# Kernel tuning notes

Measured on AMD Instinct MI355X. Metric: run time of the kernel, lower is better.

Reference implementation:

```python
import jax, jax.numpy as jnp
import numpy as np

B, Tin, Tout = 256, 32, 29
Venc, Vdec = 29, 72
E = 256; H = 256; L = 3; G = 4 * H; D = 2 * L  # bidirectional dirs * layers


def lstm_step(x, h, c, Wih0, Wih1, Whh, b):
    """One timestep of a 3-layer bidirectional LSTM (torch gate order i,f,g,o).
    x: [B, in], h/c: [D, B, H] in torch layout (layer-major, dir-minor)."""
    new_h, new_c = [], []
    inp = x
    for l in range(L):
        outs = []
        for d in range(2):
            idx = 2 * l + d
            Wih = Wih0[d] if l == 0 else Wih1[l - 1, d]
            g = inp @ Wih.T + h[idx] @ Whh[l, d].T + b[l, d]
            i_g, f_g, g_g, o_g = jnp.split(g, 4, axis=-1)
            cc = jax.nn.sigmoid(f_g) * c[idx] + jax.nn.sigmoid(i_g) * jnp.tanh(g_g)
            hh = jax.nn.sigmoid(o_g) * jnp.tanh(cc)
            new_h.append(hh); new_c.append(cc); outs.append(hh)
        inp = jnp.concatenate(outs, axis=-1)  # feeds next layer: [B, 2H]
    return jnp.stack(new_h), jnp.stack(new_c), inp


def proj(hid, W1, b1, W2, b2):
    """Linear over hidden dim then Linear over the layer*dir dim -- the exact
    math of torch's linear1 -> permute(2,1,0) -> linear2 -> permute(2,1,0)."""
    hn = jnp.einsum('lbh,gh->lbg', hid, W1) + b1            # [D, B, H]
    return jnp.einsum('lbh,ml->mbh', hn, W2) + b2[:, None, None]


def setup_inputs() -> dict:
    key = jax.random.key(0)
    ks = iter(jax.random.split(key, 64))
    def p(shape, scale=0.06):
        return jax.random.normal(next(ks), shape, jnp.float32) * scale
    return {
        "input": jax.random.randint(next(ks), (B, Tin), 0, Venc),
        "target": jax.random.randint(next(ks), (B, Tout), 0, Vdec),
        "teacher_force": 1,
        "enc_emb": p((Venc, E)), "dec_emb": p((Vdec, E)),
        "enc_Wih0": p((2, G, E)), "enc_Wih1": p((L - 1, 2, G, 2 * H)),
        "enc_Whh": p((L, 2, G, H)), "enc_b": p((L, 2, G)),
        "dec_Wih0": p((2, G, E)), "dec_Wih1": p((L - 1, 2, G, 2 * H)),
        "dec_Whh": p((L, 2, G, H)), "dec_b": p((L, 2, G)),
        "lin_h_W1": p((H, H)), "lin_h_b1": p((H,)), "lin_h_W2": p((D, D)), "lin_h_b2": p((D,)),
        "lin_c_W1": p((H, H)), "lin_c_b1": p((H,)), "lin_c_W2": p((D, D)), "lin_c_b2": p((D,)),
        "lin_a_W1": p((H, H)), "lin_a_b1": p((H,)), "lin_a_W2": p((D, D)), "lin_a_b2": p((D,)),
        "attn_W": p((E, E + H)), "attn_b": p((E,)),
        "fc_W": p((Vdec, 2 * H)), "fc_b": p((Vdec,)),
    }


def reference(input, target, teacher_force, enc_emb, dec_emb, enc_Wih0, enc_Wih1, enc_Whh, enc_b, dec_Wih0, dec_Wih1, dec_Whh, dec_b, lin_h_W1, lin_h_b1, lin_h_W2, lin_h_b2, lin_c_W1, lin_c_b1, lin_c_W2, lin_c_b2, lin_a_W1, lin_a_b1, lin_a_W2, lin_a_b2, attn_W, attn_b, fc_W, fc_b):
    Bb = input.shape[0]
    h0 = jnp.zeros((D, Bb, H), jnp.float32)

    # ---- encoder: step LSTM over Tin, projecting hidden per step for attention ----
    def enc_step(carry, x_t):
        h, c = carry
        h, c, _ = lstm_step(enc_emb[x_t], h, c, enc_Wih0, enc_Wih1, enc_Whh, enc_b)
        return (h, c), proj(h, lin_a_W1, lin_a_b1, lin_a_W2, lin_a_b2)

    (h, c), encoder_outputs = jax.lax.scan(enc_step, (h0, h0), input.T)  # [Tin, D, B, H]

    # ---- encoder->decoder state bridging (linear over H, linear over D) ----
    dec_h = proj(h, lin_h_W1, lin_h_b1, lin_h_W2, lin_h_b2)
    dec_c = proj(c, lin_c_W1, lin_c_b1, lin_c_W2, lin_c_b2)

    def dec_core(h, c, tok):
        emb = dec_emb[tok]                                # [B, E]
        energies = h[None] * encoder_outputs              # [Tin, D, B, H]
        aw = jax.nn.softmax(energies, axis=0)             # attn over source time
        ctx = (aw * encoder_outputs).sum(0).mean(0)       # [B, H]
        x = jnp.concatenate([emb, ctx], -1) @ attn_W.T + attn_b
        h, c, top = lstm_step(x, h, c, dec_Wih0, dec_Wih1, dec_Whh, dec_b)
        return h, c, top @ fc_W.T + fc_b, aw.sum(-1)      # logits [B,V], aw [Tin,D,B]

    if teacher_force:
        def step(carry, tok):
            h, c = carry
            h, c, logits, _ = dec_core(h, c, tok)
            return (h, c), logits
        _, logits_seq = jax.lax.scan(step, (dec_h, dec_c), target[:, :Tout - 1].T)
        attn_seq = jnp.zeros((Tout - 1, Tin, D, Bb), jnp.float32)
    else:
        def step(carry, _):
            h, c, tok = carry
            h, c, logits, aw = dec_core(h, c, tok)
            nxt = jnp.argmax(jax.nn.softmax(logits, -1), -1).astype(tok.dtype)
            return (h, c, nxt), (logits, aw)
        tok0 = jnp.ones((Bb,), input.dtype)
        _, (logits_seq, attn_seq) = jax.lax.scan(step, (dec_h, dec_c, tok0), None, length=Tout - 1)

    pred0 = jnp.zeros((1, Bb, Vdec), jnp.float32).at[0, :, 1].set(1.0)
    predicted = jnp.concatenate([pred0, logits_seq], 0)   # [Tout, B, Vdec]
    attn_weights = jnp.concatenate([jnp.zeros((1, Tin, D, Bb), jnp.float32), attn_seq], 0)
    return predicted, attn_weights
```

## Files before the change

kernel.cpp:

```cpp
#include <hip/hip_runtime.h>
#include <math.h>

#define BB 256
#define TIN 32
#define TOUT 29
#define VDEC 72
#define EDIM 256
#define HDIM 256
#define DD 6
#define BH (BB*HDIM)

typedef unsigned short u16;
typedef unsigned int u32;
typedef __bf16 bf16x8 __attribute__((ext_vector_type(8)));
typedef float f32x4 __attribute__((ext_vector_type(4)));
typedef u16 u16x8 __attribute__((ext_vector_type(8)));

__device__ __forceinline__ float sigmf(float x){ return 1.0f/(1.0f+__expf(-x)); }
__device__ __forceinline__ float tanhf_fast(float x){ return 1.0f - 2.0f/(1.0f+__expf(2.0f*x)); }
__device__ __forceinline__ u16 f2bf(float f){
  u32 u = __builtin_bit_cast(u32, f);
  u32 r = (u + 0x7fffu + ((u>>16)&1u)) >> 16;
  return (u16)r;
}
__device__ __forceinline__ float bf2f(u16 s){
  u32 u = ((u32)s)<<16; return __builtin_bit_cast(float, u);
}
__device__ __forceinline__ bf16x8 ldbf8(const u16* p){
  u16x8 t = *(const u16x8*)p; return __builtin_bit_cast(bf16x8, t);
}
__device__ __forceinline__ f32x4 mfma16(bf16x8 a, bf16x8 b, f32x4 c){
  return __builtin_amdgcn_mfma_f32_16x16x32_bf16(a, b, c, 0, 0, 0);
}

__global__ void fill_zero_u32(u32* __restrict__ p, int n){
  int i = blockIdx.x*256 + threadIdx.x;
  if (i < n) p[i] = 0u;
}

__global__ void init_out_kernel(float* __restrict__ out, int n){
  int i = blockIdx.x*256 + threadIdx.x;
  if (i >= n) return;
  float v = 0.0f;
  if (i < BB*VDEC && (i % VDEC) == 1) v = 1.0f;
  out[i] = v;
}

__global__ void bias2d_kernel(const float* __restrict__ W2a, const float* __restrict__ b1a, const float* __restrict__ b2a,
                              const float* __restrict__ W2h, const float* __restrict__ b1h, const float* __restrict__ b2h,
                              const float* __restrict__ W2c, const float* __restrict__ b1c, const float* __restrict__ b2c,
                              float* __restrict__ outp){
  int g = threadIdx.x;
  const float* W2[3] = {W2a, W2h, W2c};
  const float* b1[3] = {b1a, b1h, b1c};
  const float* b2[3] = {b2a, b2h, b2c};
  for (int p = 0; p < 3; p++)
    for (int m = 0; m < 6; m++){
      float s = 0.f;
      for (int l = 0; l < 6; l++) s += W2[p][m*6+l];
      outp[p*1536 + m*256 + g] = s * b1[p][g] + b2[p][m];
    }
}

__global__ void embed_enc_kernel(const int* __restrict__ input, const float* __restrict__ enc_emb,
                                 u16* __restrict__ x_emb){
  int i = blockIdx.x*256 + threadIdx.x;
  int e = i & 255, b = (i >> 8) & 255, t = i >> 16;
  x_emb[i] = f2bf(enc_emb[(size_t)input[b*TIN + t]*EDIM + e]);
}

__global__ void pack_w_kernel(const float* __restrict__ Wih, const float* __restrict__ Whh,
                              u16* __restrict__ dst, int K1, int K){
  int k = blockIdx.x*256 + threadIdx.x;
  int row = blockIdx.y;
  int d = row >> 10, rr = row & 1023;
  int ht = rr >> 6, r = rr & 63;
  int g = (r>>4)*256 + ht*16 + (r&15);
  float v;
  if (k < K1) v = Wih[((size_t)d*1024 + g)*K1 + k];
  else        v = Whh[((size_t)d*1024 + g)*256 + (k - K1)];
  dst[(size_t)row*K + k] = f2bf(v);
}

__global__ void pack_wfused_kernel(const float* __restrict__ Wih0, const float* __restrict__ attn_W,
                                   const float* __restrict__ Whh, u16* __restrict__ dst){
  int k = blockIdx.x*256 + threadIdx.x;
  int row = blockIdx.y;
  int d = row >> 10, rr = row & 1023;
  int ht = rr >> 6, r = rr & 63;
  int g = (r>>4)*256 + ht*16 + (r&15);
  float v;
  if (k >= 512) v = Whh[((size_t)d*1024 + g)*256 + (k - 512)];
  else {
    const float* wr = Wih0 + ((size_t)d*1024 + g)*256;
    float s = 0.f;
    #pragma unroll 4
    for (int o = 0; o < 256; o++) s += wr[o] * attn_W[(size_t)o*512 + k];
    v = s;
  }
  dst[(size_t)row*768 + k] = f2bf(v);
}

__global__ void biasfold_kernel(const float* __restrict__ Wih0, const float* __restrict__ attn_b,
                                const float* __restrict__ dec_b, float* __restrict__ outb){
  int i = blockIdx.x*256 + threadIdx.x;
  int d = i >> 10, g = i & 1023;
  const float* wr = Wih0 + ((size_t)d*1024 + g)*256;
  float s = dec_b[d*1024 + g];
  #pragma unroll 4
  for (int o = 0; o < 256; o++) s += wr[o]*attn_b[o];
  outb[i] = s;
}

__global__ void mix_kernel(const float* __restrict__ inp, float* __restrict__ outp,
                           const float* __restrict__ W2, int n){
  int i = blockIdx.x*256 + threadIdx.x;
  if (i >= n) return;
  int h = i & 255, b = (i >> 8) & 255, t = i >> 16;
  size_t base = ((size_t)t*6)*BH + (size_t)b*256 + h;
  float v[6];
  #pragma unroll
  for (int l = 0; l < 6; l++) v[l] = inp[base + (size_t)l*BH];
  #pragma unroll
  for (int m = 0; m < 6; m++){
    float s = 0.f;
    #pragma unroll
    for (int l = 0; l < 6; l++) s += W2[m*6+l]*v[l];
    outp[base + (size_t)m*BH] = s;
  }
}

__global__ __launch_bounds__(256) void gemmN256_kernel(const float* __restrict__ A, float* __restrict__ C,
                                                       const float* __restrict__ W,
                                                       const float* __restrict__ bias2d,
                                                       u16* __restrict__ Cbf){
  __shared__ float As[32][33];
  __shared__ float Ws[256][34];
  int tid = threadIdx.x;
  int m_base = blockIdx.x * 32;
  int rg = tid >> 5, cg = tid & 31;
  float acc[4][8];
  #pragma unroll
  for (int i=0;i<4;i++)
    #pragma unroll
    for (int j=0;j<8;j++) acc[i][j]=0.f;
  for (int k0 = 0; k0 < 256; k0 += 32){
    #pragma unroll
    for (int p=0;p<4;p++) As[rg + p*8][cg] = A[(size_t)(m_base + rg + p*8)*256 + k0 + cg];
    #pragma unroll
    for (int p=0;p<32;p++) Ws[rg + p*8][cg] = W[(size_t)(rg + p*8)*256 + k0 + cg];
    __syncthreads();
    #pragma unroll
    for (int kk=0; kk<32; kk++){
      float a[4], w[8];
      #pragma unroll
      for (int i=0;i<4;i++) a[i] = As[rg*4+i][kk];
      #pragma unroll
      for (int j=0;j<8;j++) w[j] = Ws[cg*8+j][kk];
      #pragma unroll
      for (int i=0;i<4;i++)
        #pragma unroll
        for (int j=0;j<8;j++) acc[i][j] += a[i]*w[j];
    }
    __syncthreads();
  }
  #pragma unroll
  for (int i=0;i<4;i++){
    int row = m_base + rg*4 + i;
    int bm = (row >> 8) % 6;
    #pragma unroll
    for (int j=0;j<8;j++){
      float v = acc[i][j] + bias2d[bm*256 + cg*8 + j];
      if (C)   C[(size_t)row*256 + cg*8 + j] = v;
      if (Cbf) Cbf[(size_t)row*256 + cg*8 + j] = f2bf(v);
    }
  }
}

template<int K1>
__global__ __launch_bounds__(256) void lstm_stage_mfma(
    const u16* __restrict__ inp,
    const u16* __restrict__ Wpk,
    const float* __restrict__ bias_l,
    const u16* __restrict__ hR, u16* __restrict__ hW,
    float* __restrict__ cBuf, u16* __restrict__ inp_out,
    float* __restrict__ h_all_t, int l){
  constexpr int K = K1 + 256;
  constexpr int NIT = K >> 6;
  __shared__ __align__(16) u16 As[2][32][72];
  __shared__ __align__(16) u16 Ws[2][64][72];
  __shared__ float Gt[4][32][17];
  int tid = threadIdx.x;
  int m_base = blockIdx.x*32;
  int d = blockIdx.y >> 4, ht = blockIdx.y & 15;
  int idx = 2*l + d;
  const u16* Wblk = Wpk + (size_t)((d*16+ht)*64)*K;
  int q = tid >> 6, lane = tid & 63;
  int ar = tid >> 3, kp = (tid & 7)*8;
  const u16* aRow  = inp + (size_t)(m_base+ar)*K1 + kp;
  const u16* hRow  = hR + (size_t)idx*BH + (size_t)(m_base+ar)*HDIM + kp - K1;
  const u16* wRow0 = Wblk + (size_t)ar*K + kp;
  const u16* wRow1 = Wblk + (size_t)(ar+32)*K + kp;
  uint4 aP[2], w0P[2], w1P[2];
  #pragma unroll
  for (int pf = 0; pf < 2; pf++){
    int c0 = pf*64;
    const u16* ap = (c0 + kp < K1) ? aRow : hRow;
    aP[pf]  = *(const uint4*)(ap + c0);
    w0P[pf] = *(const uint4*)(wRow0 + c0);
    w1P[pf] = *(const uint4*)(wRow1 + c0);
  }
  f32x4 acc0 = {0.f,0.f,0.f,0.f}, acc1 = {0.f,0.f,0.f,0.f};
  #pragma unroll
  for (int i = 0; i < NIT; i++){
    int p = i & 1;
    *(uint4*)&As[p][ar][kp]     = aP[p];
    *(uint4*)&Ws[p][ar][kp]     = w0P[p];
    *(uint4*)&Ws[p][ar+32][kp]  = w1P[p];
    int c0n = (i+2) << 6;
    if (c0n < K){
      const u16* ap = (c0n + kp < K1) ? aRow : hRow;
      aP[p]  = *(const uint4*)(ap + c0n);
      w0P[p] = *(const uint4*)(wRow0 + c0n);
      w1P[p] = *(const uint4*)(wRow1 + c0n);
    }
    __syncthreads();
    #pragma unroll
    for (int kh = 0; kh < 2; kh++){
      int kb = kh*32 + (lane>>4)*8;
      bf16x8 a0 = ldbf8(&As[p][lane & 15][kb]);
      bf16x8 a1 = ldbf8(&As[p][16 + (lane & 15)][kb]);
      bf16x8 bq = ldbf8(&Ws[p][q*16 + (lane & 15)][kb]);
      acc0 = mfma16(a0, bq, acc0);
      acc1 = mfma16(a1, bq, acc1);
    }
  }
  int hh = lane & 15, rq = lane >> 4;
  #pragma unroll
  for (int r = 0; r < 4; r++){
    Gt[q][rq*4 + r][hh]      = acc0[r];
    Gt[q][16 + rq*4 + r][hh] = acc1[r];
  }
  __syncthreads();
  const float* bias = bias_l + d*1024;
  #pragma unroll
  for (int it = 0; it < 2; it++){
    int id = tid + it*256;
    int bb = id >> 4, h2 = id & 15;
    int b = m_base + bb, h = ht*16 + h2;
    float iv = Gt[0][bb][h2] + bias[h];
    float fv = Gt[1][bb][h2] + bias[256 + h];
    float gv = Gt[2][bb][h2] + bias[512 + h];
    float ov = Gt[3][bb][h2] + bias[768 + h];
    size_t off = (size_t)idx*BH + (size_t)b*HDIM + h;
    float cold = cBuf[off];
    float cc = sigmf(fv)*cold + sigmf(iv)*tanhf_fast(gv);
    float hv = sigmf(ov)*tanhf_fast(cc);
    cBuf[off] = cc;
    u16 hb = f2bf(hv);
    hW[off] = hb;
    inp_out[(size_t)b*512 + d*HDIM + h] = hb;
    if (h_all_t) h_all_t[off] = hv;
  }
}

__global__ void attn_tok_kernel(const u16* __restrict__ hR, const u16* __restrict__ eo,
                                u16* __restrict__ cat, const int* __restrict__ tf,
                                float* __restrict__ attn_out, int step,
                                const int* __restrict__ target, float* __restrict__ outp,
                                const float* __restrict__ dec_emb, const u16* __restrict__ top,
                                const float* __restrict__ fc_W, const float* __restrict__ fc_b){
  int blk = blockIdx.x, tid = threadIdx.x;
  __shared__ float s[512];
  __shared__ float lg[VDEC];
  __shared__ int tokS;
  if (blk < 256){
    int b = blk, hc = tid;
    bool wa = (tf[0] == 0);
    float acc = 0.f;
    for (int d = 0; d < DD; d++){
      float hv = bf2f(hR[(size_t)d*BH + (size_t)b*256 + hc]);
      const u16* ep = eo + (size_t)d*BH + (size_t)b*256 + hc;
      float se = 0.f, ac = 0.f;
      #pragma unroll 8
      for (int t = 0; t < TIN; t++){
        float ev = bf2f(ep[(size_t)t*(DD*BH)]);
        float e = __expf(hv*ev);
        se += e; ac += e*ev;
      }
      acc += ac/se;
      if (wa){
        float inv = 1.f/se;
        for (int t = 0; t < TIN; t++){
          float ev = bf2f(ep[(size_t)t*(DD*BH)]);
          atomicAdd(&attn_out[(((size_t)(step+1)*TIN + t)*DD + d)*BB + b], __expf(hv*ev)*inv);
        }
      }
    }
    cat[(size_t)b*512 + 256 + hc] = f2bf(acc*(1.0f/6.0f));
  } else {
    int b = blk - 256;
    if (step > 0){
      s[tid]       = bf2f(top[(size_t)b*512 + tid]);
      s[tid + 256] = bf2f(top[(size_t)b*512 + 256 + tid]);
      __syncthreads();
      if (tid < VDEC){
        float a = fc_b[tid];
        #pragma unroll 4
        for (int k = 0; k < 512; k++) a += s[k]*fc_W[(size_t)tid*512 + k];
        outp[((size_t)step*BB + b)*VDEC + tid] = a;
        lg[tid] = a;
      }
      __syncthreads();
    }
    int tok;
    if (tf[0]) tok = target[b*TOUT + step];
    else if (step == 0) tok = 1;
    else {
      if (tid == 0){
        int bi = 0; float bv = lg[0];
        for (int v = 1; v < VDEC; v++){ float x = lg[v]; if (x > bv){ bv = x; bi = v; } }
        tokS = bi;
      }
      __syncthreads();
      tok = tokS;
    }
    cat[(size_t)b*512 + tid] = f2bf(dec_emb[(size_t)tok*EDIM + tid]);
  }
}

__global__ void fc_kernel(const u16* __restrict__ top, const float* __restrict__ fc_W,
                          const float* __restrict__ fc_b, float* __restrict__ outp, int step){
  __shared__ float s[512];
  int b = blockIdx.x, tid = threadIdx.x;
  s[tid]       = bf2f(top[(size_t)b*512 + tid]);
  s[tid + 256] = bf2f(top[(size_t)b*512 + 256 + tid]);
  __syncthreads();
  if (tid < VDEC){
    float a = fc_b[tid];
    #pragma unroll 4
    for (int k = 0; k < 512; k++) a += s[k]*fc_W[(size_t)tid*512 + k];
    outp[((size_t)(step+1)*BB + b)*VDEC + tid] = a;
  }
}


extern "C" void kernel_launch(void* const* d_in, const int* in_sizes, int n_in,
                              void* d_out, int out_size, void* d_ws, size_t ws_size,
                              hipStream_t stream){
  (void)in_sizes; (void)n_in; (void)out_size; (void)ws_size;
  const int*   input    = (const int*)d_in[0];
  const int*   target   = (const int*)d_in[1];
  const int*   tf       = (const int*)d_in[2];
  const float* enc_emb  = (const float*)d_in[3];
  const float* dec_emb  = (const float*)d_in[4];
  const float* enc_Wih0 = (const float*)d_in[5];
  const float* enc_Wih1 = (const float*)d_in[6];
  const float* enc_Whh  = (const float*)d_in[7];
  const float* enc_b    = (const float*)d_in[8];
  const float* dec_Wih0 = (const float*)d_in[9];
  const float* dec_Wih1 = (const float*)d_in[10];
  const float* dec_Whh  = (const float*)d_in[11];
  const float* dec_b    = (const float*)d_in[12];
  const float* lin_h_W1 = (const float*)d_in[13];
  const float* lin_h_b1 = (const float*)d_in[14];
  const float* lin_h_W2 = (const float*)d_in[15];
  const float* lin_h_b2 = (const float*)d_in[16];
  const float* lin_c_W1 = (const float*)d_in[17];
  const float* lin_c_b1 = (const float*)d_in[18];
  const float* lin_c_W2 = (const float*)d_in[19];
  const float* lin_c_b2 = (const float*)d_in[20];
  const float* lin_a_W1 = (const float*)d_in[21];
  const float* lin_a_b1 = (const float*)d_in[22];
  const float* lin_a_W2 = (const float*)d_in[23];
  const float* lin_a_b2 = (const float*)d_in[24];
  const float* attn_W   = (const float*)d_in[25];
  const float* attn_b   = (const float*)d_in[26];
  const float* fc_W     = (const float*)d_in[27];
  const float* fc_b     = (const float*)d_in[28];
  float* out = (float*)d_out;

  char* base = (char*)d_ws;
  size_t off = 0;
  auto alloc = [&](size_t bytes)->char*{
    char* p = base + off; off += (bytes + 255) & ~(size_t)255; return p;
  };
  float* h_all  = (float*)alloc(sizeof(float)*(size_t)TIN*DD*BH);
  float* tmp6   = (float*)alloc(sizeof(float)*(size_t)DD*BH);
  float* dec_c  = (float*)alloc(sizeof(float)*(size_t)DD*BH);
  float* bias2d = (float*)alloc(sizeof(float)*3*6*256);
  u16*   enc_hA = (u16*)alloc(sizeof(u16)*(size_t)DD*BH + sizeof(float)*(size_t)DD*BH);
  float* enc_c  = (float*)(enc_hA + (size_t)DD*BH);
  u16* enc_hB = (u16*)alloc(sizeof(u16)*(size_t)DD*BH);
  u16* dec_hA = (u16*)alloc(sizeof(u16)*(size_t)DD*BH);
  u16* dec_hB = (u16*)alloc(sizeof(u16)*(size_t)DD*BH);
  u16* x_emb  = (u16*)alloc(sizeof(u16)*(size_t)TIN*BB*EDIM);
  u16* bufA   = (u16*)alloc(sizeof(u16)*(size_t)BB*512);
  u16* bufB   = (u16*)alloc(sizeof(u16)*(size_t)BB*512);
  u16* cat    = (u16*)alloc(sizeof(u16)*(size_t)BB*512);
  u16* eo_bf  = (u16*)alloc(sizeof(u16)*(size_t)TIN*DD*BH);
  u16* wp_e0  = (u16*)alloc(sizeof(u16)*(size_t)2048*512);
  u16* wp_e1  = (u16*)alloc(sizeof(u16)*(size_t)2048*768);
  u16* wp_e2  = (u16*)alloc(sizeof(u16)*(size_t)2048*768);
  u16* wp_d0f = (u16*)alloc(sizeof(u16)*(size_t)2048*768);
  u16* wp_d1  = (u16*)alloc(sizeof(u16)*(size_t)2048*768);
  u16* wp_d2  = (u16*)alloc(sizeof(u16)*(size_t)2048*768);
  float* fb0  = (float*)alloc(sizeof(float)*2048);

  const int outn = TOUT*BB*VDEC + TOUT*TIN*DD*BB;
  init_out_kernel<<<(outn+255)/256, 256, 0, stream>>>(out, outn);
  fill_zero_u32<<<(DD*BH*6/4 + 255)/256, 256, 0, stream>>>((u32*)enc_hA, DD*BH*6/4);
  bias2d_kernel<<<1, 256, 0, stream>>>(lin_a_W2, lin_a_b1, lin_a_b2,
                                       lin_h_W2, lin_h_b1, lin_h_b2,
                                       lin_c_W2, lin_c_b1, lin_c_b2, bias2d);
  embed_enc_kernel<<<(TIN*BB*EDIM)/256, 256, 0, stream>>>(input, enc_emb, x_emb);
  pack_w_kernel<<<dim3(2,2048), 256, 0, stream>>>(enc_Wih0, enc_Whh,                       wp_e0, 256, 512);
  pack_w_kernel<<<dim3(3,2048), 256, 0, stream>>>(enc_Wih1, enc_Whh + 2*1024*256,          wp_e1, 512, 768);
  pack_w_kernel<<<dim3(3,2048), 256, 0, stream>>>(enc_Wih1 + (size_t)2*1024*512, enc_Whh + 4*1024*256, wp_e2, 512, 768);
  pack_wfused_kernel<<<dim3(3,2048), 256, 0, stream>>>(dec_Wih0, attn_W, dec_Whh,          wp_d0f);
  biasfold_kernel<<<8, 256, 0, stream>>>(dec_Wih0, attn_b, dec_b, fb0);
  pack_w_kernel<<<dim3(3,2048), 256, 0, stream>>>(dec_Wih1, dec_Whh + 2*1024*256,          wp_d1, 512, 768);
  pack_w_kernel<<<dim3(3,2048), 256, 0, stream>>>(dec_Wih1 + (size_t)2*1024*512, dec_Whh + 4*1024*256, wp_d2, 512, 768);

  dim3 sgrid(8, 32);
  for (int t = 0; t < TIN; t++){
    const u16* hRb = (t & 1) ? enc_hB : enc_hA;
    u16*       hWb = (t & 1) ? enc_hA : enc_hB;
    float* hat = h_all + (size_t)t*DD*BH;
    lstm_stage_mfma<256><<<sgrid,256,0,stream>>>(x_emb + (size_t)t*BB*EDIM, wp_e0,
        enc_b,        hRb, hWb, enc_c, bufA, hat, 0);
    lstm_stage_mfma<512><<<sgrid,256,0,stream>>>(bufA, wp_e1,
        enc_b + 2048, hRb, hWb, enc_c, bufB, hat, 1);
    lstm_stage_mfma<512><<<sgrid,256,0,stream>>>(bufB, wp_e2,
        enc_b + 4096, hRb, hWb, enc_c, bufA, hat, 2);
  }
  mix_kernel<<<BH/256, 256, 0, stream>>>(h_all + (size_t)31*DD*BH, tmp6, lin_h_W2, BH);
  gemmN256_kernel<<<(DD*BB)/32, 256, 0, stream>>>(tmp6, nullptr, lin_h_W1, bias2d + 1536, dec_hA);
  mix_kernel<<<BH/256, 256, 0, stream>>>(enc_c, tmp6, lin_c_W2, BH);
  gemmN256_kernel<<<(DD*BB)/32, 256, 0, stream>>>(tmp6, dec_c, lin_c_W1, bias2d + 3072, nullptr);
  mix_kernel<<<(TIN*BH)/256, 256, 0, stream>>>(h_all, h_all, lin_a_W2, TIN*BH);
  gemmN256_kernel<<<(TIN*DD*BB)/32, 256, 0, stream>>>(h_all, nullptr, lin_a_W1, bias2d, eo_bf);

  float* attn_out = out + (size_t)TOUT*BB*VDEC;
  for (int i = 0; i < TOUT-1; i++){
    const u16* hRb = (i & 1) ? dec_hB : dec_hA;
    u16*       hWb = (i & 1) ? dec_hA : dec_hB;
    attn_tok_kernel<<<512, 256, 0, stream>>>(hRb, eo_bf, cat, tf, attn_out, i,
                                             target, out, dec_emb, bufA, fc_W, fc_b);
    lstm_stage_mfma<512><<<sgrid,256,0,stream>>>(cat,  wp_d0f,
        fb0,          hRb, hWb, dec_c, bufA, nullptr, 0);
    lstm_stage_mfma<512><<<sgrid,256,0,stream>>>(bufA, wp_d1,
        dec_b + 2048, hRb, hWb, dec_c, bufB, nullptr, 1);
    lstm_stage_mfma<512><<<sgrid,256,0,stream>>>(bufB, wp_d2,
        dec_b + 4096, hRb, hWb, dec_c, bufA, nullptr, 2);
  }
  fc_kernel<<<BB, 256, 0, stream>>>(bufA, fc_W, fc_b, out, TOUT-2);
}
```

Baseline: 3.751 ms.

## Fuse encoder/decoder stages into persistent mega-kernel with software grid barriers

Replaces about 200 sequential kernel launches (per-timestep LSTM stages, attention/token, mix, GEMM, final fc) with one persistent 256-block kernel. Phases are separated by a custom atomic grid barrier, and shared memory is reused through a union. The attention/token work now runs in the same blocks, and the fc dot product is split three ways per vocab entry. The goal is to remove launch overhead and inter-kernel gaps, at the cost of relying on all 256 blocks being co-resident and on barrier spin cost.

```diff
diff --git a/kernel.cpp b/kernel.cpp
--- a/kernel.cpp
+++ b/kernel.cpp
@@ -9,6 +9,7 @@
 #define HDIM 256
 #define DD 6
 #define BH (BB*HDIM)
+#define NBLK 256
 
 typedef unsigned short u16;
 typedef unsigned int u32;
@@ -31,6 +32,29 @@
 }
 __device__ __forceinline__ f32x4 mfma16(bf16x8 a, bf16x8 b, f32x4 c){
   return __builtin_amdgcn_mfma_f32_16x16x32_bf16(a, b, c, 0, 0, 0);
+}
+
+union SharedU {
+  struct { u16 As[2][32][72]; u16 Ws[2][64][72]; float Gt[4][32][17]; } st;
+  struct { float As[32][33]; float Ws[256][34]; } gm;
+  struct { float s[512]; float p3[VDEC][3]; float lg[VDEC]; int tok; } fc;
+};
+
+__device__ __forceinline__ void gridbar(u32* __restrict__ arr, u32* __restrict__ gen,
+                                        u32 g, int bid){
+  __syncthreads();
+  if (threadIdx.x == 0)
+    __hip_atomic_store(&arr[bid], g, __ATOMIC_RELEASE, __HIP_MEMORY_SCOPE_AGENT);
+  if (bid == 0){
+    while (__hip_atomic_load(&arr[threadIdx.x], __ATOMIC_RELAXED, __HIP_MEMORY_SCOPE_AGENT) < g) {}
+    __syncthreads();
+    if (threadIdx.x == 0)
+      __hip_atomic_store(gen, g, __ATOMIC_RELEASE, __HIP_MEMORY_SCOPE_AGENT);
+  } else if (threadIdx.x == 0){
+    while (__hip_atomic_load(gen, __ATOMIC_RELAXED, __HIP_MEMORY_SCOPE_AGENT) < g) {}
+  }
+  __builtin_amdgcn_fence(__ATOMIC_ACQUIRE, "agent");
+  __syncthreads();
 }
 
 __global__ void fill_zero_u32(u32* __restrict__ p, int n){
@@ -112,87 +136,18 @@
   outb[i] = s;
 }
 
-__global__ void mix_kernel(const float* __restrict__ inp, float* __restrict__ outp,
-                           const float* __restrict__ W2, int n){
-  int i = blockIdx.x*256 + threadIdx.x;
-  if (i >= n) return;
-  int h = i & 255, b = (i >> 8) & 255, t = i >> 16;
-  size_t base = ((size_t)t*6)*BH + (size_t)b*256 + h;
-  float v[6];
-  #pragma unroll
-  for (int l = 0; l < 6; l++) v[l] = inp[base + (size_t)l*BH];
-  #pragma unroll
-  for (int m = 0; m < 6; m++){
-    float s = 0.f;
-    #pragma unroll
-    for (int l = 0; l < 6; l++) s += W2[m*6+l]*v[l];
-    outp[base + (size_t)m*BH] = s;
-  }
-}
-
-__global__ __launch_bounds__(256) void gemmN256_kernel(const float* __restrict__ A, float* __restrict__ C,
-                                                       const float* __restrict__ W,
-                                                       const float* __restrict__ bias2d,
-                                                       u16* __restrict__ Cbf){
-  __shared__ float As[32][33];
-  __shared__ float Ws[256][34];
-  int tid = threadIdx.x;
-  int m_base = blockIdx.x * 32;
-  int rg = tid >> 5, cg = tid & 31;
-  float acc[4][8];
-  #pragma unroll
-  for (int i=0;i<4;i++)
-    #pragma unroll
-    for (int j=0;j<8;j++) acc[i][j]=0.f;
-  for (int k0 = 0; k0 < 256; k0 += 32){
-    #pragma unroll
-    for (int p=0;p<4;p++) As[rg + p*8][cg] = A[(size_t)(m_base + rg + p*8)*256 + k0 + cg];
-    #pragma unroll
-    for (int p=0;p<32;p++) Ws[rg + p*8][cg] = W[(size_t)(rg + p*8)*256 + k0 + cg];
-    __syncthreads();
-    #pragma unroll
-    for (int kk=0; kk<32; kk++){
-      float a[4], w[8];
-      #pragma unroll
-      for (int i=0;i<4;i++) a[i] = As[rg*4+i][kk];
-      #pragma unroll
-      for (int j=0;j<8;j++) w[j] = Ws[cg*8+j][kk];
-      #pragma unroll
-      for (int i=0;i<4;i++)
-        #pragma unroll
-        for (int j=0;j<8;j++) acc[i][j] += a[i]*w[j];
-    }
-    __syncthreads();
-  }
-  #pragma unroll
-  for (int i=0;i<4;i++){
-    int row = m_base + rg*4 + i;
-    int bm = (row >> 8) % 6;
-    #pragma unroll
-    for (int j=0;j<8;j++){
-      float v = acc[i][j] + bias2d[bm*256 + cg*8 + j];
-      if (C)   C[(size_t)row*256 + cg*8 + j] = v;
-      if (Cbf) Cbf[(size_t)row*256 + cg*8 + j] = f2bf(v);
-    }
-  }
-}
-
 template<int K1>
-__global__ __launch_bounds__(256) void lstm_stage_mfma(
-    const u16* __restrict__ inp,
-    const u16* __restrict__ Wpk,
-    const float* __restrict__ bias_l,
-    const u16* __restrict__ hR, u16* __restrict__ hW,
-    float* __restrict__ cBuf, u16* __restrict__ inp_out,
-    float* __restrict__ h_all_t, int l){
+__device__ __forceinline__ void stage_phase(SharedU* shp, int bid,
+    const u16* __restrict__ inp, const u16* __restrict__ Wpk, const float* __restrict__ bias_l,
+    const u16* __restrict__ hR, u16* __restrict__ hW, float* __restrict__ cBuf,
+    u16* __restrict__ inp_out, float* __restrict__ h_all_t, int l){
+  auto& ss = shp->st;
   constexpr int K = K1 + 256;
   constexpr int NIT = K >> 6;
-  __shared__ __align__(16) u16 As[2][32][72];
-  __shared__ __align__(16) u16 Ws[2][64][72];
-  __shared__ float Gt[4][32][17];
   int tid = threadIdx.x;
-  int m_base = blockIdx.x*32;
-  int d = blockIdx.y >> 4, ht = blockIdx.y & 15;
+  int m_base = (bid >> 5) * 32;
+  int y = bid & 31;
+  int d = y >> 4, ht = y & 15;
   int idx = 2*l + d;
   const u16* Wblk = Wpk + (size_t)((d*16+ht)*64)*K;
   int q = tid >> 6, lane = tid & 63;
@@ -214,9 +169,9 @@
   #pragma unroll
   for (int i = 0; i < NIT; i++){
     int p = i & 1;
-    *(uint4*)&As[p][ar][kp]     = aP[p];
-    *(uint4*)&Ws[p][ar][kp]     = w0P[p];
-    *(uint4*)&Ws[p][ar+32][kp]  = w1P[p];
+    *(uint4*)&ss.As[p][ar][kp]     = aP[p];
+    *(uint4*)&ss.Ws[p][ar][kp]     = w0P[p];
+    *(uint4*)&ss.Ws[p][ar+32][kp]  = w1P[p];
     int c0n = (i+2) << 6;
     if (c0n < K){
       const u16* ap = (c0n + kp < K1) ? aRow : hRow;
@@ -228,9 +183,9 @@
     #pragma unroll
     for (int kh = 0; kh < 2; kh++){
       int kb = kh*32 + (lane>>4)*8;
-      bf16x8 a0 = ldbf8(&As[p][lane & 15][kb]);
-      bf16x8 a1 = ldbf8(&As[p][16 + (lane & 15)][kb]);
-      bf16x8 bq = ldbf8(&Ws[p][q*16 + (lane & 15)][kb]);
+      bf16x8 a0 = ldbf8(&ss.As[p][lane & 15][kb]);
+      bf16x8 a1 = ldbf8(&ss.As[p][16 + (lane & 15)][kb]);
+      bf16x8 bq = ldbf8(&ss.Ws[p][q*16 + (lane & 15)][kb]);
       acc0 = mfma16(a0, bq, acc0);
       acc1 = mfma16(a1, bq, acc1);
     }
@@ -238,8 +193,8 @@
   int hh = lane & 15, rq = lane >> 4;
   #pragma unroll
   for (int r = 0; r < 4; r++){
-    Gt[q][rq*4 + r][hh]      = acc0[r];
-    Gt[q][16 + rq*4 + r][hh] = acc1[r];
+    ss.Gt[q][rq*4 + r][hh]      = acc0[r];
+    ss.Gt[q][16 + rq*4 + r][hh] = acc1[r];
   }
   __syncthreads();
   const float* bias = bias_l + d*1024;
@@ -248,10 +203,10 @@
     int id = tid + it*256;
     int bb = id >> 4, h2 = id & 15;
     int b = m_base + bb, h = ht*16 + h2;
-    float iv = Gt[0][bb][h2] + bias[h];
-    float fv = Gt[1][bb][h2] + bias[256 + h];
-    float gv = Gt[2][bb][h2] + bias[512 + h];
-    float ov = Gt[3][bb][h2] + bias[768 + h];
+    float iv = ss.Gt[0][bb][h2] + bias[h];
+    float fv = ss.Gt[1][bb][h2] + bias[256 + h];
+    float gv = ss.Gt[2][bb][h2] + bias[512 + h];
+    float ov = ss.Gt[3][bb][h2] + bias[768 + h];
     size_t off = (size_t)idx*BH + (size_t)b*HDIM + h;
     float cold = cBuf[off];
     float cc = sigmf(fv)*cold + sigmf(iv)*tanhf_fast(gv);
@@ -264,84 +219,216 @@
   }
 }
 
-__global__ void attn_tok_kernel(const u16* __restrict__ hR, const u16* __restrict__ eo,
-                                u16* __restrict__ cat, const int* __restrict__ tf,
-                                float* __restrict__ attn_out, int step,
-                                const int* __restrict__ target, float* __restrict__ outp,
-                                const float* __restrict__ dec_emb, const u16* __restrict__ top,
-                                const float* __restrict__ fc_W, const float* __restrict__ fc_b){
-  int blk = blockIdx.x, tid = threadIdx.x;
-  __shared__ float s[512];
-  __shared__ float lg[VDEC];
-  __shared__ int tokS;
-  if (blk < 256){
-    int b = blk, hc = tid;
-    bool wa = (tf[0] == 0);
-    float acc = 0.f;
-    for (int d = 0; d < DD; d++){
-      float hv = bf2f(hR[(size_t)d*BH + (size_t)b*256 + hc]);
-      const u16* ep = eo + (size_t)d*BH + (size_t)b*256 + hc;
-      float se = 0.f, ac = 0.f;
-      #pragma unroll 8
+__device__ __forceinline__ void mix_phase(int bid, const float* __restrict__ inp,
+    float* __restrict__ outp, const float* __restrict__ W2, int n){
+  for (int i = bid*256 + (int)threadIdx.x; i < n; i += NBLK*256){
+    int h = i & 255, b = (i >> 8) & 255, t = i >> 16;
+    size_t base2 = ((size_t)t*6)*BH + (size_t)b*256 + h;
+    float v[6];
+    #pragma unroll
+    for (int l = 0; l < 6; l++) v[l] = inp[base2 + (size_t)l*BH];
+    #pragma unroll
+    for (int m = 0; m < 6; m++){
+      float s = 0.f;
+      #pragma unroll
+      for (int l = 0; l < 6; l++) s += W2[m*6+l]*v[l];
+      outp[base2 + (size_t)m*BH] = s;
+    }
+  }
+}
+
+__device__ __forceinline__ void gemm_tile(SharedU* shp, int m_base,
+    const float* __restrict__ A, float* __restrict__ C, const float* __restrict__ W,
+    const float* __restrict__ bias2d, u16* __restrict__ Cbf){
+  auto& sg = shp->gm;
+  int tid = threadIdx.x;
+  int rg = tid >> 5, cg = tid & 31;
+  float acc[4][8];
+  #pragma unroll
+  for (int i=0;i<4;i++)
+    #pragma unroll
+    for (int j=0;j<8;j++) acc[i][j]=0.f;
+  for (int k0 = 0; k0 < 256; k0 += 32){
+    #pragma unroll
+    for (int p=0;p<4;p++) sg.As[rg + p*8][cg] = A[(size_t)(m_base + rg + p*8)*256 + k0 + cg];
+    #pragma unroll
+    for (int p=0;p<32;p++) sg.Ws[rg + p*8][cg] = W[(size_t)(rg + p*8)*256 + k0 + cg];
+    __syncthreads();
+    #pragma unroll
+    for (int kk=0; kk<32; kk++){
+      float a[4], w[8];
+      #pragma unroll
+      for (int i=0;i<4;i++) a[i] = sg.As[rg*4+i][kk];
+      #pragma unroll
+      for (int j=0;j<8;j++) w[j] = sg.Ws[cg*8+j][kk];
+      #pragma unroll
+      for (int i=0;i<4;i++)
+        #pragma unroll
+        for (int j=0;j<8;j++) acc[i][j] += a[i]*w[j];
+    }
+    __syncthreads();
+  }
+  #pragma unroll
+  for (int i=0;i<4;i++){
+    int row = m_base + rg*4 + i;
+    int bm = (row >> 8) % 6;
+    #pragma unroll
+    for (int j=0;j<8;j++){
+      float v = acc[i][j] + bias2d[bm*256 + cg*8 + j];
+      if (C)   C[(size_t)row*256 + cg*8 + j] = v;
+      if (Cbf) Cbf[(size_t)row*256 + cg*8 + j] = f2bf(v);
+    }
+  }
+}
+
+__device__ __forceinline__ void attn_phase(SharedU* shp, int b, int step,
+    const u16* __restrict__ hR, const u16* __restrict__ eo, u16* __restrict__ cat,
+    const int* __restrict__ tf, float* __restrict__ attn_out,
+    const int* __restrict__ target, float* __restrict__ outp,
+    const float* __restrict__ dec_emb, const u16* __restrict__ top,
+    const float* __restrict__ fc_W, const float* __restrict__ fc_b){
+  auto& sf = shp->fc;
+  int tid = threadIdx.x;
+  if (step > 0){
+    sf.s[tid]       = bf2f(top[(size_t)b*512 + tid]);
+    sf.s[tid + 256] = bf2f(top[(size_t)b*512 + 256 + tid]);
+    __syncthreads();
+    if (tid < 3*VDEC){
+      int v = tid/3, part = tid - 3*(tid/3);
+      int k0 = part*171, k1 = (part==2) ? 512 : (k0+171);
+      const float* wr = fc_W + (size_t)v*512;
+      float a = 0.f;
+      for (int k = k0; k < k1; k++) a += sf.s[k]*wr[k];
+      sf.p3[v][part] = a;
+    }
+    __syncthreads();
+    if (tid < VDEC){
+      float a = fc_b[tid] + sf.p3[tid][0] + sf.p3[tid][1] + sf.p3[tid][2];
+      outp[((size_t)step*BB + b)*VDEC + tid] = a;
+      sf.lg[tid] = a;
+    }
+    __syncthreads();
+  }
+  int tok;
+  if (tf[0]) tok = target[b*TOUT + step];
+  else if (step == 0) tok = 1;
+  else {
+    if (tid == 0){
+      int bi = 0; float bv = sf.lg[0];
+      for (int v = 1; v < VDEC; v++){ float x = sf.lg[v]; if (x > bv){ bv = x; bi = v; } }
+      sf.tok = bi;
+    }
+    __syncthreads();
+    tok = sf.tok;
+  }
+  cat[(size_t)b*512 + tid] = f2bf(dec_emb[(size_t)tok*EDIM + tid]);
+  int hc = tid;
+  bool wa = (tf[0] == 0);
+  float acc = 0.f;
+  for (int d = 0; d < DD; d++){
+    float hv = bf2f(hR[(size_t)d*BH + (size_t)b*256 + hc]);
+    const u16* ep = eo + (size_t)d*BH + (size_t)b*256 + hc;
+    float se = 0.f, ac = 0.f;
+    #pragma unroll 8
+    for (int t = 0; t < TIN; t++){
+      float ev = bf2f(ep[(size_t)t*(DD*BH)]);
+      float e = __expf(hv*ev);
+      se += e; ac += e*ev;
+    }
+    acc += ac/se;
+    if (wa){
+      float inv = 1.f/se;
       for (int t = 0; t < TIN; t++){
         float ev = bf2f(ep[(size_t)t*(DD*BH)]);
-        float e = __expf(hv*ev);
-        se += e; ac += e*ev;
+        atomicAdd(&attn_out[(((size_t)(step+1)*TIN + t)*DD + d)*BB + b], __expf(hv*ev)*inv);
       }
-      acc += ac/se;
-      if (wa){
-        float inv = 1.f/se;
-        for (int t = 0; t < TIN; t++){
-          float ev = bf2f(ep[(size_t)t*(DD*BH)]);
-          atomicAdd(&attn_out[(((size_t)(step+1)*TIN + t)*DD + d)*BB + b], __expf(hv*ev)*inv);
-        }
-      }
-    }
-    cat[(size_t)b*512 + 256 + hc] = f2bf(acc*(1.0f/6.0f));
-  } else {
-    int b = blk - 256;
-    if (step > 0){
-      s[tid]       = bf2f(top[(size_t)b*512 + tid]);
-      s[tid + 256] = bf2f(top[(size_t)b*512 + 256 + tid]);
-      __syncthreads();
-      if (tid < VDEC){
-        float a = fc_b[tid];
-        #pragma unroll 4
-        for (int k = 0; k < 512; k++) a += s[k]*fc_W[(size_t)tid*512 + k];
-        outp[((size_t)step*BB + b)*VDEC + tid] = a;
-        lg[tid] = a;
-      }
-      __syncthreads();
-    }
-    int tok;
-    if (tf[0]) tok = target[b*TOUT + step];
-    else if (step == 0) tok = 1;
-    else {
-      if (tid == 0){
-        int bi = 0; float bv = lg[0];
-        for (int v = 1; v < VDEC; v++){ float x = lg[v]; if (x > bv){ bv = x; bi = v; } }
-        tokS = bi;
-      }
-      __syncthreads();
-      tok = tokS;
-    }
-    cat[(size_t)b*512 + tid] = f2bf(dec_emb[(size_t)tok*EDIM + tid]);
-  }
-}
-
-__global__ void fc_kernel(const u16* __restrict__ top, const float* __restrict__ fc_W,
-                          const float* __restrict__ fc_b, float* __restrict__ outp, int step){
-  __shared__ float s[512];
-  int b = blockIdx.x, tid = threadIdx.x;
-  s[tid]       = bf2f(top[(size_t)b*512 + tid]);
-  s[tid + 256] = bf2f(top[(size_t)b*512 + 256 + tid]);
+    }
+  }
+  cat[(size_t)b*512 + 256 + hc] = f2bf(acc*(1.0f/6.0f));
+}
+
+__device__ __forceinline__ void fc_final_phase(SharedU* shp, int b,
+    const u16* __restrict__ top, const float* __restrict__ fc_W,
+    const float* __restrict__ fc_b, float* __restrict__ outp){
+  auto& sf = shp->fc;
+  int tid = threadIdx.x;
+  sf.s[tid]       = bf2f(top[(size_t)b*512 + tid]);
+  sf.s[tid + 256] = bf2f(top[(size_t)b*512 + 256 + tid]);
+  __syncthreads();
+  if (tid < 3*VDEC){
+    int v = tid/3, part = tid - 3*(tid/3);
+    int k0 = part*171, k1 = (part==2) ? 512 : (k0+171);
+    const float* wr = fc_W + (size_t)v*512;
+    float a = 0.f;
+    for (int k = k0; k < k1; k++) a += sf.s[k]*wr[k];
+    sf.p3[v][part] = a;
+  }
   __syncthreads();
   if (tid < VDEC){
-    float a = fc_b[tid];
-    #pragma unroll 4
-    for (int k = 0; k < 512; k++) a += s[k]*fc_W[(size_t)tid*512 + k];
-    outp[((size_t)(step+1)*BB + b)*VDEC + tid] = a;
-  }
+    float a = fc_b[tid] + sf.p3[tid][0] + sf.p3[tid][1] + sf.p3[tid][2];
+    outp[((size_t)(TOUT-1)*BB + b)*VDEC + tid] = a;
+  }
+}
+
+__global__ __launch_bounds__(256, 1) void mega_kernel(
+    const int* __restrict__ target, const int* __restrict__ tf,
+    const float* __restrict__ dec_emb, const u16* __restrict__ x_emb,
+    const u16* __restrict__ wp_e0, const u16* __restrict__ wp_e1, const u16* __restrict__ wp_e2,
+    const u16* __restrict__ wp_d0f, const u16* __restrict__ wp_d1, const u16* __restrict__ wp_d2,
+    const float* __restrict__ enc_b, const float* __restrict__ dec_b, const float* __restrict__ fb0,
+    const float* __restrict__ lin_h_W1, const float* __restrict__ lin_c_W1, const float* __restrict__ lin_a_W1,
+    const float* __restrict__ lin_h_W2, const float* __restrict__ lin_c_W2, const float* __restrict__ lin_a_W2,
+    const float* __restrict__ bias2d,
+    const float* __restrict__ fc_W, const float* __restrict__ fc_b,
+    float* __restrict__ out,
+    float* __restrict__ h_all, float* __restrict__ tmp6, float* __restrict__ tmp6c,
+    float* __restrict__ dec_c, u16* __restrict__ enc_hA, float* __restrict__ enc_c,
+    u16* __restrict__ enc_hB, u16* __restrict__ dec_hA, u16* __restrict__ dec_hB,
+    u16* __restrict__ bufA, u16* __restrict__ bufB, u16* __restrict__ cat,
+    u16* __restrict__ eo_bf, u32* __restrict__ bar_arr, u32* __restrict__ bar_gen)
+{
+  __shared__ SharedU sh;
+  int bid = blockIdx.x;
+  u32 g = 0;
+
+  for (int t = 0; t < TIN; t++){
+    const u16* hRb = (t & 1) ? enc_hB : enc_hA;
+    u16*       hWb = (t & 1) ? enc_hA : enc_hB;
+    float* hat = h_all + (size_t)t*DD*BH;
+    stage_phase<256>(&sh, bid, x_emb + (size_t)t*BB*EDIM, wp_e0, enc_b,        hRb, hWb, enc_c, bufA, hat, 0);
+    gridbar(bar_arr, bar_gen, ++g, bid);
+    stage_phase<512>(&sh, bid, bufA,                      wp_e1, enc_b + 2048, hRb, hWb, enc_c, bufB, hat, 1);
+    gridbar(bar_arr, bar_gen, ++g, bid);
+    stage_phase<512>(&sh, bid, bufB,                      wp_e2, enc_b + 4096, hRb, hWb, enc_c, bufA, hat, 2);
+    gridbar(bar_arr, bar_gen, ++g, bid);
+  }
+
+  mix_phase(bid, h_all + (size_t)31*DD*BH, tmp6,  lin_h_W2, BH);
+  mix_phase(bid, enc_c,                    tmp6c, lin_c_W2, BH);
+  gridbar(bar_arr, bar_gen, ++g, bid);
+  if (bid < 48)       gemm_tile(&sh, bid*32,      tmp6,  nullptr, lin_h_W1, bias2d + 1536, dec_hA);
+  else if (bid < 96)  gemm_tile(&sh, (bid-48)*32, tmp6c, dec_c,   lin_c_W1, bias2d + 3072, nullptr);
+  gridbar(bar_arr, bar_gen, ++g, bid);
+  mix_phase(bid, h_all, h_all, lin_a_W2, TIN*BH);
+  gridbar(bar_arr, bar_gen, ++g, bid);
+  for (int tile = bid; tile < 1536; tile += NBLK)
+    gemm_tile(&sh, tile*32, h_all, nullptr, lin_a_W1, bias2d, eo_bf);
+  gridbar(bar_arr, bar_gen, ++g, bid);
+
+  float* attn_out = out + (size_t)TOUT*BB*VDEC;
+  for (int i = 0; i < TOUT-1; i++){
+    const u16* hRb = (i & 1) ? dec_hB : dec_hA;
+    u16*       hWb = (i & 1) ? dec_hA : dec_hB;
+    attn_phase(&sh, bid, i, hRb, eo_bf, cat, tf, attn_out, target, out, dec_emb, bufA, fc_W, fc_b);
+    gridbar(bar_arr, bar_gen, ++g, bid);
+    stage_phase<512>(&sh, bid, cat,  wp_d0f, fb0,          hRb, hWb, dec_c, bufA, nullptr, 0);
+    gridbar(bar_arr, bar_gen, ++g, bid);
+    stage_phase<512>(&sh, bid, bufA, wp_d1,  dec_b + 2048, hRb, hWb, dec_c, bufB, nullptr, 1);
+    gridbar(bar_arr, bar_gen, ++g, bid);
+    stage_phase<512>(&sh, bid, bufB, wp_d2,  dec_b + 4096, hRb, hWb, dec_c, bufA, nullptr, 2);
+    gridbar(bar_arr, bar_gen, ++g, bid);
+  }
+  fc_final_phase(&sh, bid, bufA, fc_W, fc_b, out);
 }
 
 
@@ -387,6 +474,7 @@
   };
   float* h_all  = (float*)alloc(sizeof(float)*(size_t)TIN*DD*BH);
   float* tmp6   = (float*)alloc(sizeof(float)*(size_t)DD*BH);
+  float* tmp6c  = (float*)alloc(sizeof(float)*(size_t)DD*BH);
   float* dec_c  = (float*)alloc(sizeof(float)*(size_t)DD*BH);
   float* bias2d = (float*)alloc(sizeof(float)*3*6*256);
   u16*   enc_hA = (u16*)alloc(sizeof(u16)*(size_t)DD*BH + sizeof(float)*(size_t)DD*BH);
@@ -406,10 +494,12 @@
   u16* wp_d1  = (u16*)alloc(sizeof(u16)*(size_t)2048*768);
   u16* wp_d2  = (u16*)alloc(sizeof(u16)*(size_t)2048*768);
   float* fb0  = (float*)alloc(sizeof(float)*2048);
+  u32* barblk = (u32*)alloc(sizeof(u32)*512);
 
   const int outn = TOUT*BB*VDEC + TOUT*TIN*DD*BB;
   init_out_kernel<<<(outn+255)/256, 256, 0, stream>>>(out, outn);
   fill_zero_u32<<<(DD*BH*6/4 + 255)/256, 256, 0, stream>>>((u32*)enc_hA, DD*BH*6/4);
+  fill_zero_u32<<<2, 256, 0, stream>>>(barblk, 512);
   bias2d_kernel<<<1, 256, 0, stream>>>(lin_a_W2, lin_a_b1, lin_a_b2,
                                        lin_h_W2, lin_h_b1, lin_h_b2,
                                        lin_c_W2, lin_c_b1, lin_c_b2, bias2d);
@@ -422,37 +512,12 @@
   pack_w_kernel<<<dim3(3,2048), 256, 0, stream>>>(dec_Wih1, dec_Whh + 2*1024*256,          wp_d1, 512, 768);
   pack_w_kernel<<<dim3(3,2048), 256, 0, stream>>>(dec_Wih1 + (size_t)2*1024*512, dec_Whh + 4*1024*256, wp_d2, 512, 768);
 
-  dim3 sgrid(8, 32);
-  for (int t = 0; t < TIN; t++){
-    const u16* hRb = (t & 1) ? enc_hB : enc_hA;
-    u16*       hWb = (t & 1) ? enc_hA : enc_hB;
-    float* hat = h_all + (size_t)t*DD*BH;
-    lstm_stage_mfma<256><<<sgrid,256,0,stream>>>(x_emb + (size_t)t*BB*EDIM, wp_e0,
-        enc_b,        hRb, hWb, enc_c, bufA, hat, 0);
-    lstm_stage_mfma<512><<<sgrid,256,0,stream>>>(bufA, wp_e1,
-        enc_b + 2048, hRb, hWb, enc_c, bufB, hat, 1);
-    lstm_stage_mfma<512><<<sgrid,256,0,stream>>>(bufB, wp_e2,
-        enc_b + 4096, hRb, hWb, enc_c, bufA, hat, 2);
-  }
-  mix_kernel<<<BH/256, 256, 0, stream>>>(h_all + (size_t)31*DD*BH, tmp6, lin_h_W2, BH);
-  gemmN256_kernel<<<(DD*BB)/32, 256, 0, stream>>>(tmp6, nullptr, lin_h_W1, bias2d + 1536, dec_hA);
-  mix_kernel<<<BH/256, 256, 0, stream>>>(enc_c, tmp6, lin_c_W2, BH);
-  gemmN256_kernel<<<(DD*BB)/32, 256, 0, stream>>>(tmp6, dec_c, lin_c_W1, bias2d + 3072, nullptr);
-  mix_kernel<<<(TIN*BH)/256, 256, 0, stream>>>(h_all, h_all, lin_a_W2, TIN*BH);
-  gemmN256_kernel<<<(TIN*DD*BB)/32, 256, 0, stream>>>(h_all, nullptr, lin_a_W1, bias2d, eo_bf);
-
-  float* attn_out = out + (size_t)TOUT*BB*VDEC;
-  for (int i = 0; i < TOUT-1; i++){
-    const u16* hRb = (i & 1) ? dec_hB : dec_hA;
-    u16*       hWb = (i & 1) ? dec_hA : dec_hB;
-    attn_tok_kernel<<<512, 256, 0, stream>>>(hRb, eo_bf, cat, tf, attn_out, i,
-                                             target, out, dec_emb, bufA, fc_W, fc_b);
-    lstm_stage_mfma<512><<<sgrid,256,0,stream>>>(cat,  wp_d0f,
-        fb0,          hRb, hWb, dec_c, bufA, nullptr, 0);
-    lstm_stage_mfma<512><<<sgrid,256,0,stream>>>(bufA, wp_d1,
-        dec_b + 2048, hRb, hWb, dec_c, bufB, nullptr, 1);
-    lstm_stage_mfma<512><<<sgrid,256,0,stream>>>(bufB, wp_d2,
-        dec_b + 4096, hRb, hWb, dec_c, bufA, nullptr, 2);
-  }
-  fc_kernel<<<BB, 256, 0, stream>>>(bufA, fc_W, fc_b, out, TOUT-2);
-}
+  mega_kernel<<<NBLK, 256, 0, stream>>>(
+      target, tf, dec_emb, x_emb,
+      wp_e0, wp_e1, wp_e2, wp_d0f, wp_d1, wp_d2,
+      enc_b, dec_b, fb0,
+      lin_h_W1, lin_c_W1, lin_a_W1, lin_h_W2, lin_c_W2, lin_a_W2,
+      bias2d, fc_W, fc_b, out,
+      h_all, tmp6, tmp6c, dec_c, enc_hA, enc_c, enc_hB, dec_hA, dec_hB,
+      bufA, bufB, cat, eo_bf, barblk, barblk + 256);
+}
```

Result: slower. 8.950 ms (+138.6%).
